# Kernel tuning notes

Hardware: AMD Instinct MI355X
Metric: run time of the kernel (lower is better)

## Reference

```python
import jax, jax.numpy as jnp
import numpy as np

B, NP, FIN = 128, 64, 2048   # graphs, nodes per graph, input feat
H, D = 8, 64                 # GAT heads, per-head dim
HD = H * D                   # 512
HID = 1024                   # Set2Set channels (concat of two 512 convs)
R2 = 16.0                    # radius^2 (r=4)
SLOPE = 0.2                  # GATConv leaky_relu slope
EPS = 0.1                    # BatchNorm eps


def setup_inputs() -> dict:
    key = jax.random.key(0)
    ks = jax.random.split(key, 20)
    s = 0.02
    inp = {}
    inp['x'] = jax.random.normal(ks[0], (B * NP, FIN), jnp.float32)
    inp['pos'] = jax.random.uniform(ks[1], (B * NP, 2), jnp.float32) * 20.0
    inp['batch'] = jnp.repeat(jnp.arange(B, dtype=jnp.int32), NP)
    # lin01: Linear(2048,2048,bias=False) + BN(2048, eps=0.1) (eval mode)
    inp['W0'] = jax.random.normal(ks[2], (FIN, 2048), jnp.float32) * s
    inp['bn0_g'] = jnp.ones((2048,), jnp.float32)
    inp['bn0_b'] = jnp.zeros((2048,), jnp.float32)
    inp['bn0_m'] = jnp.zeros((2048,), jnp.float32)
    inp['bn0_v'] = jnp.ones((2048,), jnp.float32)
    # two GATConv(2048, 64, heads=8)
    inp['Wg1'] = jax.random.normal(ks[3], (2048, HD), jnp.float32) * s
    inp['as1'] = jax.random.normal(ks[4], (H, D), jnp.float32) * s
    inp['ad1'] = jax.random.normal(ks[5], (H, D), jnp.float32) * s
    inp['b1'] = jnp.zeros((HD,), jnp.float32)
    inp['Wg2'] = jax.random.normal(ks[6], (2048, HD), jnp.float32) * s
    inp['as2'] = jax.random.normal(ks[7], (H, D), jnp.float32) * s
    inp['ad2'] = jax.random.normal(ks[8], (H, D), jnp.float32) * s
    inp['b2'] = jnp.zeros((HD,), jnp.float32)
    # Set2Set LSTM: 2 layers, input 2*HID, hidden HID
    inp['Wih0'] = jax.random.normal(ks[9], (4 * HID, 2 * HID), jnp.float32) * s
    inp['Whh0'] = jax.random.normal(ks[10], (4 * HID, HID), jnp.float32) * s
    inp['bih0'] = jnp.zeros((4 * HID,), jnp.float32)
    inp['bhh0'] = jnp.zeros((4 * HID,), jnp.float32)
    inp['Wih1'] = jax.random.normal(ks[11], (4 * HID, HID), jnp.float32) * s
    inp['Whh1'] = jax.random.normal(ks[12], (4 * HID, HID), jnp.float32) * s
    inp['bih1'] = jnp.zeros((4 * HID,), jnp.float32)
    inp['bhh1'] = jnp.zeros((4 * HID,), jnp.float32)
    # lin2: Linear(2048,1024,bias=False) + BN(1024, eps=0.1)
    inp['W2'] = jax.random.normal(ks[13], (2 * HID, HID), jnp.float32) * s
    inp['bn2_g'] = jnp.ones((HID,), jnp.float32)
    inp['bn2_b'] = jnp.zeros((HID,), jnp.float32)
    inp['bn2_m'] = jnp.zeros((HID,), jnp.float32)
    inp['bn2_v'] = jnp.ones((HID,), jnp.float32)
    # lin3: Linear(1024, 10)
    inp['W3'] = jax.random.normal(ks[14], (HID, 10), jnp.float32) * s
    inp['b3'] = jnp.zeros((10,), jnp.float32)
    return inp


def _bn(x, g, b, m, v):
    return (x - m) * jax.lax.rsqrt(v + EPS) * g + b


def _gat(xb, adj, Wg, a_src, a_dst, bias):
    # xb: [B, NP, 2048], adj: [B, NP, NP] bool (diag True = self-loops)
    h = (xb @ Wg).reshape(B, NP, H, D)
    es = jnp.einsum('bnhd,hd->bnh', h, a_src)   # source-node score
    ed = jnp.einsum('bnhd,hd->bnh', h, a_dst)   # target-node score
    # e[b, i, j, h]: edge j -> i
    e = jax.nn.leaky_relu(ed[:, :, None, :] + es[:, None, :, :], SLOPE)
    e = jnp.where(adj[..., None], e, -jnp.inf)
    alpha = jax.nn.softmax(e, axis=2)           # softmax over neighbors j
    out = jnp.einsum('bijh,bjhd->bihd', alpha, h).reshape(B, NP, HD)
    return out + bias


def _cell(inp, h, c, Wih, Whh, bih, bhh):
    z = inp @ Wih.T + h @ Whh.T + bih + bhh
    i, f, g, o = jnp.split(z, 4, axis=-1)
    c = jax.nn.sigmoid(f) * c + jax.nn.sigmoid(i) * jnp.tanh(g)
    return jax.nn.sigmoid(o) * jnp.tanh(c), c


def _forward(x, pos, W0, bn0_g, bn0_b, bn0_m, bn0_v,
             Wg1, as1, ad1, b1, Wg2, as2, ad2, b2,
             Wih0, Whh0, bih0, bhh0, Wih1, Whh1, bih1, bhh1,
             W2, bn2_g, bn2_b, bn2_m, bn2_v, W3, b3):
    # radius_graph(r=4) per graph; GATConv re-adds self-loops -> diag True
    p = pos.reshape(B, NP, 2)
    d2 = jnp.sum((p[:, :, None, :] - p[:, None, :, :]) ** 2, axis=-1)
    adj = d2 <= R2
    x = _bn(jax.nn.relu(x @ W0), bn0_g, bn0_b, bn0_m, bn0_v)  # dropout: eval
    xb = x.reshape(B, NP, 2048)
    g1 = jax.nn.relu(_gat(xb, adj, Wg1, as1, ad1, b1))
    g2 = jax.nn.relu(_gat(xb, adj, Wg2, as2, ad2, b2))
    x2 = jnp.concatenate([g1, g2], axis=-1)                   # [B, NP, 1024]
    # Set2Set: processing_steps=2, 2-layer LSTM
    q_star = jnp.zeros((B, 2 * HID), x2.dtype)
    h0 = c0 = h1 = c1 = jnp.zeros((B, HID), x2.dtype)
    for _ in range(2):
        h0, c0 = _cell(q_star, h0, c0, Wih0, Whh0, bih0, bhh0)
        h1, c1 = _cell(h0, h1, c1, Wih1, Whh1, bih1, bhh1)
        e = jnp.einsum('bnd,bd->bn', x2, h1)
        a = jax.nn.softmax(e, axis=1)                         # per-graph softmax
        r = jnp.einsum('bn,bnd->bd', a, x2)
        q_star = jnp.concatenate([h1, r], axis=-1)            # [B, 2048]
    y = _bn(jax.nn.relu(q_star @ W2), bn2_g, bn2_b, bn2_m, bn2_v)
    return y @ W3 + b3                                        # [B, 10] ('A2')


def reference(x, pos, batch, W0, bn0_g, bn0_b, bn0_m, bn0_v,
              Wg1, as1, ad1, b1, Wg2, as2, ad2, b2,
              Wih0, Whh0, bih0, bhh0, Wih1, Whh1, bih1, bhh1,
              W2, bn2_g, bn2_b, bn2_m, bn2_v, W3, b3):
    # batch ids are implicit in the fixed [B, NP] layout
    return _forward(x, pos, W0, bn0_g, bn0_b, bn0_m, bn0_v,
                    Wg1, as1, ad1, b1, Wg2, as2, ad2, b2,
                    Wih0, Whh0, bih0, bhh0, Wih1, Whh1, bih1, bhh1,
                    W2, bn2_g, bn2_b, bn2_m, bn2_v, W3, b3)
```

## Files before the change

### kernel.cpp

```cpp
#include <hip/hip_runtime.h>
#include <hip/hip_bf16.h>

typedef unsigned short u16;
typedef __attribute__((ext_vector_type(8))) short short8;
typedef __attribute__((ext_vector_type(4))) float f32x4;
typedef unsigned long long u64;

#define DI __device__ __forceinline__

DI u16 f2b(float f){
  unsigned u = __float_as_uint(f);
  unsigned r = 0x7fffu + ((u >> 16) & 1u);
  return (u16)((u + r) >> 16);
}
DI float b2f(u16 u){ return __uint_as_float((unsigned)u << 16); }

DI void gl_lds16(const void* g, void* l){
  __builtin_amdgcn_global_load_lds((const __attribute__((address_space(1))) void*)g,
                                   (__attribute__((address_space(3))) void*)l, 16, 0, 0);
}

constexpr size_t O_XBF = 0;
constexpr size_t O_W0T = O_XBF + 33554432;
constexpr size_t O_WGT = O_W0T + 8388608;
constexpr size_t O_W2T = O_WGT + 4194304;
constexpr size_t O_XB  = O_W2T + 4194304;
constexpr size_t O_H   = O_XB  + 33554432;
constexpr size_t O_ES  = O_H   + 33554432;
constexpr size_t O_ED  = O_ES  + 524288;
constexpr size_t O_ADJ = O_ED  + 524288;
constexpr size_t O_SC0 = O_ADJ + 65536;
constexpr size_t O_SH0 = O_SC0 + 8192;
constexpr size_t O_SC2 = O_SH0 + 8192;
constexpr size_t O_SH2 = O_SC2 + 4096;
constexpr size_t O_LB0 = O_SH2 + 4096;
constexpr size_t O_LB1 = O_LB0 + 16384;
constexpr size_t S_AC0 = 0;
constexpr size_t S_AC1 = S_AC0 + 786432;
constexpr size_t S_C0  = S_AC1 + 524288;
constexpr size_t S_C1  = S_C0  + 524288;
constexpr size_t S_H1F = S_C1  + 524288;
constexpr size_t S_ZP  = S_H1F + 524288;
constexpr size_t S_E   = S_ZP  + 16777216;
constexpr size_t S_Z1U = S_E   + 32768;

__global__ __launch_bounds__(256) void cvt_x(const float* __restrict__ x, u16* __restrict__ xbf){
  int idx = blockIdx.x * 256 + threadIdx.x;
  int r = idx >> 9, c4 = (idx & 511) << 2;
  float4 v = *(const float4*)(x + (size_t)r * 2048 + c4);
  u16 o[4] = { f2b(v.x), f2b(v.y), f2b(v.z), f2b(v.w) };
  *(ushort4*)(xbf + (size_t)r * 2048 + c4) = *(ushort4*)o;
}

__global__ void cvt_tr(const float* __restrict__ W0, const float* __restrict__ Wg1,
                       const float* __restrict__ Wg2, const float* __restrict__ W2,
                       u16* __restrict__ w0t, u16* __restrict__ wgt, u16* __restrict__ w2t){
  __shared__ float tile[32][33];
  int bx = blockIdx.x;
  const float* src; u16* dst; int C, droff;
  if(bx < 64){      src = W0;  dst = w0t; C = 2048; droff = 0; }
  else if(bx < 80){ src = Wg1; dst = wgt; C = 512;  droff = 0;   bx -= 64; }
  else if(bx < 96){ src = Wg2; dst = wgt; C = 512;  droff = 512; bx -= 80; }
  else {            src = W2;  dst = w2t; C = 1024; droff = 0;   bx -= 96; }
  int c0 = bx * 32, r0 = blockIdx.y * 32;
  int tx = threadIdx.x, ty = threadIdx.y;
  for(int i = 0; i < 4; i++)
    tile[ty + 8*i][tx] = src[(size_t)(r0 + ty + 8*i) * C + c0 + tx];
  __syncthreads();
  for(int i = 0; i < 4; i++)
    dst[(size_t)(droff + c0 + ty + 8*i) * 2048 + r0 + tx] = f2b(tile[tx][ty + 8*i]);
}

__global__ __launch_bounds__(256) void prep_adj(
    const float* __restrict__ g0, const float* __restrict__ b0, const float* __restrict__ m0, const float* __restrict__ v0,
    const float* __restrict__ g2, const float* __restrict__ b2, const float* __restrict__ m2, const float* __restrict__ v2,
    const float* __restrict__ bih0, const float* __restrict__ bhh0,
    const float* __restrict__ bih1, const float* __restrict__ bhh1,
    float* __restrict__ sc0, float* __restrict__ sh0, float* __restrict__ sc2, float* __restrict__ sh2,
    float* __restrict__ lb0, float* __restrict__ lb1,
    const float* __restrict__ pos, u64* __restrict__ adjm){
  int bx = blockIdx.x, tid = threadIdx.x;
  if(bx < 16){
    int t = bx * 256 + tid;
    if(t < 2048){ float s = g0[t] * rsqrtf(v0[t] + 0.1f); sc0[t] = s; sh0[t] = b0[t] - m0[t] * s; }
    if(t < 1024){ float s = g2[t] * rsqrtf(v2[t] + 0.1f); sc2[t] = s; sh2[t] = b2[t] - m2[t] * s; }
    lb0[t] = bih0[t] + bhh0[t];
    lb1[t] = bih1[t] + bhh1[t];
  } else {
    __shared__ float px[4][64], py[4][64];
    int w = tid >> 6, l = tid & 63;
    int g = (bx - 16) * 4 + w;
    float2 p = ((const float2*)pos)[g * 64 + l];
    px[w][l] = p.x; py[w][l] = p.y;
    __syncthreads();
    float xi = p.x, yi = p.y;
    u64 m = 0;
    for(int j = 0; j < 64; j++){
      float dx = xi - px[w][j], dy = yi - py[w][j];
      if(dx * dx + dy * dy <= 16.0f) m |= (1ull << j);
    }
    adjm[g * 64 + l] = m;
  }
}

template<int MODE>
__global__ __launch_bounds__(256) void gemm_bf16(
    const u16* __restrict__ A, const u16* __restrict__ Bt,
    float* __restrict__ Cf, u16* __restrict__ Cb,
    const float* __restrict__ p1, const float* __restrict__ p2,
    int M, int N, int K)
{
  constexpr int BM = 128, BN = 128, BK = 64;
  __shared__ alignas(16) u16 Al[BM * BK];
  __shared__ alignas(16) u16 Bl[BN * BK];
  int m0 = blockIdx.x * BM, n0 = blockIdx.y * BN;
  int t = threadIdx.x, w = t >> 6, l = t & 63;
  int wm = (w >> 1) * 64, wn = (w & 1) * 64;
  f32x4 acc[4][4];
  for(int a = 0; a < 4; a++) for(int b = 0; b < 4; b++) acc[a][b] = {0.f, 0.f, 0.f, 0.f};

  const short8* Ap = (const short8*)Al;
  const short8* Bp = (const short8*)Bl;

  for(int k0 = 0; k0 < K; k0 += BK){
    #pragma unroll
    for(int u = t; u < BM * 8; u += 256){
      int r = u >> 3, c = u & 7;
      gl_lds16(A + (size_t)(m0 + r) * K + k0 + ((c ^ (r & 7)) << 3), Al + u * 8);
    }
    #pragma unroll
    for(int u = t; u < BN * 8; u += 256){
      int r = u >> 3, c = u & 7;
      gl_lds16(Bt + (size_t)(n0 + r) * K + k0 + ((c ^ (r & 7)) << 3), Bl + u * 8);
    }
    __syncthreads();
    #pragma unroll
    for(int ks = 0; ks < 2; ks++){
      int kc = ks * 4 + (l >> 4);
      short8 av[4], bv[4];
      #pragma unroll
      for(int mi = 0; mi < 4; mi++){ int r = wm + mi * 16 + (l & 15); av[mi] = Ap[r * 8 + (kc ^ (r & 7))]; }
      #pragma unroll
      for(int ni = 0; ni < 4; ni++){ int r = wn + ni * 16 + (l & 15); bv[ni] = Bp[r * 8 + (kc ^ (r & 7))]; }
      #pragma unroll
      for(int mi = 0; mi < 4; mi++)
        #pragma unroll
        for(int ni = 0; ni < 4; ni++)
          acc[mi][ni] = __builtin_amdgcn_mfma_f32_16x16x32_bf16(av[mi], bv[ni], acc[mi][ni], 0, 0, 0);
    }
    __syncthreads();
  }

  int cr = m0 + wm + ((l >> 4) << 2);
  int cc = n0 + wn + (l & 15);
  for(int mi = 0; mi < 4; mi++)
    for(int ni = 0; ni < 4; ni++)
      for(int r = 0; r < 4; r++){
        int row = cr + mi * 16 + r, col = cc + ni * 16;
        float v = acc[mi][ni][r];
        if(MODE == 1){ v = fmaxf(v, 0.f) * p1[col] + p2[col]; Cb[(size_t)row * N + col] = f2b(v); }
        else if(MODE == 3){ Cb[(size_t)row * N + col] = f2b(v); }
        else { Cf[(size_t)row * N + col] = v; }
      }
}

__global__ __launch_bounds__(256) void gemm_sk(
    const u16* __restrict__ A, const u16* __restrict__ Bt, float* __restrict__ Cf,
    int N, int lda, int ldb, int kPer)
{
  constexpr int BM = 128, BN = 64, BK = 64;
  __shared__ alignas(16) u16 Al[BM * BK];
  __shared__ alignas(16) u16 Bl[BN * BK];
  int n0 = blockIdx.x * BN;
  int kb = blockIdx.y * kPer;
  float* C = Cf + (size_t)blockIdx.y * 128 * N;
  int t = threadIdx.x, w = t >> 6, l = t & 63;
  int wm = (w >> 1) * 64, wn = (w & 1) * 32;
  f32x4 acc[4][2];
  for(int a = 0; a < 4; a++) for(int b = 0; b < 2; b++) acc[a][b] = {0.f, 0.f, 0.f, 0.f};

  const short8* Ap = (const short8*)Al;
  const short8* Bp = (const short8*)Bl;

  for(int k0 = kb; k0 < kb + kPer; k0 += BK){
    #pragma unroll
    for(int u = t; u < BM * 8; u += 256){
      int r = u >> 3, c = u & 7;
      gl_lds16(A + (size_t)r * lda + k0 + ((c ^ (r & 7)) << 3), Al + u * 8);
    }
    #pragma unroll
    for(int u = t; u < BN * 8; u += 256){
      int r = u >> 3, c = u & 7;
      gl_lds16(Bt + (size_t)(n0 + r) * ldb + k0 + ((c ^ (r & 7)) << 3), Bl + u * 8);
    }
    __syncthreads();
    #pragma unroll
    for(int ks = 0; ks < 2; ks++){
      int kc = ks * 4 + (l >> 4);
      short8 av[4], bv[2];
      #pragma unroll
      for(int mi = 0; mi < 4; mi++){ int r = wm + mi * 16 + (l & 15); av[mi] = Ap[r * 8 + (kc ^ (r & 7))]; }
      #pragma unroll
      for(int ni = 0; ni < 2; ni++){ int r = wn + ni * 16 + (l & 15); bv[ni] = Bp[r * 8 + (kc ^ (r & 7))]; }
      #pragma unroll
      for(int mi = 0; mi < 4; mi++)
        #pragma unroll
        for(int ni = 0; ni < 2; ni++)
          acc[mi][ni] = __builtin_amdgcn_mfma_f32_16x16x32_bf16(av[mi], bv[ni], acc[mi][ni], 0, 0, 0);
    }
    __syncthreads();
  }

  int cr = wm + ((l >> 4) << 2);
  int cc = n0 + wn + (l & 15);
  for(int mi = 0; mi < 4; mi++)
    for(int ni = 0; ni < 2; ni++)
      for(int r = 0; r < 4; r++)
        C[(size_t)(cr + mi * 16 + r) * N + cc + ni * 16] = acc[mi][ni][r];
}

__global__ __launch_bounds__(256) void gemm_skf(
    const u16* __restrict__ A, const float* __restrict__ Wih, const float* __restrict__ Whh,
    float* __restrict__ Cf, int N, int lda, int Kih, int Khh, int kPer)
{
  constexpr int BM = 128, BN = 64, BK = 64;
  __shared__ alignas(16) u16 Al[BM * BK];
  __shared__ alignas(16) u16 Bl[BN * BK];
  int n0 = blockIdx.x * BN;
  int kb = blockIdx.y * kPer;
  float* C = Cf + (size_t)blockIdx.y * 128 * N;
  int t = threadIdx.x, w = t >> 6, l = t & 63;
  int wm = (w >> 1) * 64, wn = (w & 1) * 32;
  f32x4 acc[4][2];
  for(int a = 0; a < 4; a++) for(int b = 0; b < 2; b++) acc[a][b] = {0.f, 0.f, 0.f, 0.f};

  const short8* Ap = (const short8*)Al;
  const short8* Bp = (const short8*)Bl;

  for(int k0 = kb; k0 < kb + kPer; k0 += BK){
    #pragma unroll
    for(int u = t; u < BM * 8; u += 256){
      int r = u >> 3, c = u & 7;
      gl_lds16(A + (size_t)r * lda + k0 + ((c ^ (r & 7)) << 3), Al + u * 8);
    }
    #pragma unroll
    for(int u = t; u < BN * 8; u += 256){
      int r = u >> 3, c = u & 7;
      int gk = k0 + c * 8;
      const float* src = (gk < Kih) ? (Wih + (size_t)(n0 + r) * Kih + gk)
                                    : (Whh + (size_t)(n0 + r) * Khh + (gk - Kih));
      float4 v0 = *(const float4*)src;
      float4 v1 = *(const float4*)(src + 4);
      short8 ov;
      ov[0] = (short)f2b(v0.x); ov[1] = (short)f2b(v0.y); ov[2] = (short)f2b(v0.z); ov[3] = (short)f2b(v0.w);
      ov[4] = (short)f2b(v1.x); ov[5] = (short)f2b(v1.y); ov[6] = (short)f2b(v1.z); ov[7] = (short)f2b(v1.w);
      ((short8*)Bl)[r * 8 + (c ^ (r & 7))] = ov;
    }
    __syncthreads();
    #pragma unroll
    for(int ks = 0; ks < 2; ks++){
      int kc = ks * 4 + (l >> 4);
      short8 av[4], bv[2];
      #pragma unroll
      for(int mi = 0; mi < 4; mi++){ int r = wm + mi * 16 + (l & 15); av[mi] = Ap[r * 8 + (kc ^ (r & 7))]; }
      #pragma unroll
      for(int ni = 0; ni < 2; ni++){ int r = wn + ni * 16 + (l & 15); bv[ni] = Bp[r * 8 + (kc ^ (r & 7))]; }
      #pragma unroll
      for(int mi = 0; mi < 4; mi++)
        #pragma unroll
        for(int ni = 0; ni < 2; ni++)
          acc[mi][ni] = __builtin_amdgcn_mfma_f32_16x16x32_bf16(av[mi], bv[ni], acc[mi][ni], 0, 0, 0);
    }
    __syncthreads();
  }

  int cr = wm + ((l >> 4) << 2);
  int cc = n0 + wn + (l & 15);
  for(int mi = 0; mi < 4; mi++)
    for(int ni = 0; ni < 2; ni++)
      for(int r = 0; r < 4; r++)
        C[(size_t)(cr + mi * 16 + r) * N + cc + ni * 16] = acc[mi][ni][r];
}

__global__ __launch_bounds__(256) void gat_attn2(const u64* __restrict__ adjm,
    const u16* __restrict__ h,
    const float* __restrict__ as1, const float* __restrict__ ad1,
    const float* __restrict__ as2, const float* __restrict__ ad2,
    const float* __restrict__ b1, const float* __restrict__ b2,
    u16* __restrict__ x2b){
  int b = blockIdx.x;
  int cv = blockIdx.y >> 3, hh = blockIdx.y & 7;
  __shared__ float hst[64][64];
  __shared__ float alphaL[64][65];
  __shared__ float esl[64], edl[64];
  __shared__ u64 adjs[64];
  int t = threadIdx.x, w = t >> 6, l = t & 63;
  {
    int j = t >> 2, d0 = (t & 3) * 16;
    const u16* hr = h + (size_t)(b * 64 + j) * 1024 + cv * 512 + hh * 64 + d0;
    #pragma unroll
    for(int k = 0; k < 16; k++) hst[j][d0 + k] = b2f(hr[k]);
  }
  if(t < 64) adjs[t] = adjm[b * 64 + t];
  __syncthreads();
  float aSl = ((cv ? as2 : as1) + hh * 64)[l];
  float aDl = ((cv ? ad2 : ad1) + hh * 64)[l];
  for(int it = 0; it < 16; it++){
    int j = it * 4 + w;
    float v = hst[j][l];
    float ps = v * aSl, pd = v * aDl;
    for(int o = 32; o; o >>= 1){ ps += __shfl_xor(ps, o); pd += __shfl_xor(pd, o); }
    if(l == 0){ esl[j] = ps; edl[j] = pd; }
  }
  __syncthreads();
  for(int it = 0; it < 16; it++){
    int i = it * 4 + w;
    bool on = (adjs[i] >> l) & 1;
    float e = edl[i] + esl[l];
    e = e > 0.f ? e : 0.2f * e;
    float mx = on ? e : -1e30f;
    for(int o = 32; o; o >>= 1) mx = fmaxf(mx, __shfl_xor(mx, o));
    float p = on ? __expf(e - mx) : 0.f;
    float s = p;
    for(int o = 32; o; o >>= 1) s += __shfl_xor(s, o);
    alphaL[i][l] = p / s;
  }
  __syncthreads();
  int i = t >> 2, q = t & 3;
  float acc[16];
  #pragma unroll
  for(int k = 0; k < 16; k++) acc[k] = 0.f;
  for(int j = 0; j < 64; j++){
    float al = alphaL[i][j];
    const float* hr = &hst[j][q * 16];
    #pragma unroll
    for(int k = 0; k < 16; k++) acc[k] += al * hr[k];
  }
  const float* bias = (cv ? b2 : b1) + hh * 64 + q * 16;
  u16* op = x2b + (size_t)(b * 64 + i) * 1024 + cv * 512 + hh * 64 + q * 16;
  #pragma unroll
  for(int k = 0; k < 16; k++) op[k] = f2b(fmaxf(acc[k] + bias[k], 0.f));
}

__global__ __launch_bounds__(256) void s2s0_gemv(const float* __restrict__ Wih1,
    const float* __restrict__ lb1, const float* __restrict__ lb0, float* __restrict__ z1u){
  __shared__ float hs[1024];
  int t = threadIdx.x;
  for(int i = t; i < 1024; i += 256){
    float zi = lb0[i], zg = lb0[2048 + i], zo = lb0[3072 + i];
    float cn = (1.f / (1.f + __expf(-zi))) * tanhf(zg);
    hs[i] = (1.f / (1.f + __expf(-zo))) * tanhf(cn);
  }
  __syncthreads();
  int w = t >> 6, l = t & 63;
  int r = blockIdx.x * 4 + w;
  const float* wr = Wih1 + (size_t)r * 1024;
  float s = 0.f;
  #pragma unroll
  for(int k = 0; k < 16; k++) s += wr[l + 64 * k] * hs[l + 64 * k];
  for(int o = 32; o; o >>= 1) s += __shfl_xor(s, o);
  if(l == 0) z1u[r] = s + lb1[r];
}

__global__ void s2s0_bcast(const float* __restrict__ lb0, const float* __restrict__ z1u,
    float* __restrict__ c0b, float* __restrict__ c1b, float* __restrict__ h1f,
    u16* __restrict__ ac0, u16* __restrict__ ac1){
  int t = blockIdx.x * 256 + threadIdx.x;
  int b = t >> 10, j = t & 1023;
  float zi0 = lb0[j], zg0 = lb0[2048 + j], zo0 = lb0[3072 + j];
  float c0 = (1.f / (1.f + __expf(-zi0))) * tanhf(zg0);
  float h0 = (1.f / (1.f + __expf(-zo0))) * tanhf(c0);
  float zi1 = z1u[j], zg1 = z1u[2048 + j], zo1 = z1u[3072 + j];
  float c1 = (1.f / (1.f + __expf(-zi1))) * tanhf(zg1);
  float h1 = (1.f / (1.f + __expf(-zo1))) * tanhf(c1);
  c0b[t] = c0;
  c1b[t] = c1;
  h1f[t] = h1;
  u16 h0b = f2b(h0), h1b = f2b(h1);
  ac0[(size_t)b * 3072 + j] = h1b;
  ac0[(size_t)b * 3072 + 2048 + j] = h0b;
  ac1[(size_t)b * 2048 + j] = h0b;
  ac1[(size_t)b * 2048 + 1024 + j] = h1b;
}

__global__ void lstm_gate0(const float* __restrict__ zp, const float* __restrict__ lb,
                           float* __restrict__ c, u16* __restrict__ ac0, u16* __restrict__ ac1,
                           int ns){
  int t = blockIdx.x * 256 + threadIdx.x;
  int b = t >> 10, j = t & 1023;
  size_t base = (size_t)b * 4096;
  float zi = 0, zf = 0, zg = 0, zo = 0;
  for(int s = 0; s < ns; s++){
    const float* zr = zp + (size_t)s * 524288 + base;
    zi += zr[j]; zf += zr[1024 + j]; zg += zr[2048 + j]; zo += zr[3072 + j];
  }
  zi += lb[j]; zf += lb[1024 + j]; zg += lb[2048 + j]; zo += lb[3072 + j];
  float ci = c[t];
  float si = 1.f / (1.f + __expf(-zi)), sf = 1.f / (1.f + __expf(-zf)), so = 1.f / (1.f + __expf(-zo));
  float cn = sf * ci + si * tanhf(zg);
  c[t] = cn;
  u16 hb = f2b(so * tanhf(cn));
  ac0[(size_t)b * 3072 + 2048 + j] = hb;
  ac1[(size_t)b * 2048 + j] = hb;
}

__global__ void lstm_gate1(const float* __restrict__ zp, const float* __restrict__ lb,
                           float* __restrict__ c, float* __restrict__ h1f,
                           u16* __restrict__ ac1, u16* __restrict__ ac0, int ns){
  int t = blockIdx.x * 256 + threadIdx.x;
  int b = t >> 10, j = t & 1023;
  size_t base = (size_t)b * 4096;
  float zi = 0, zf = 0, zg = 0, zo = 0;
  for(int s = 0; s < ns; s++){
    const float* zr = zp + (size_t)s * 524288 + base;
    zi += zr[j]; zf += zr[1024 + j]; zg += zr[2048 + j]; zo += zr[3072 + j];
  }
  zi += lb[j]; zf += lb[1024 + j]; zg += lb[2048 + j]; zo += lb[3072 + j];
  float ci = c[t];
  float si = 1.f / (1.f + __expf(-zi)), sf = 1.f / (1.f + __expf(-zf)), so = 1.f / (1.f + __expf(-zo));
  float cn = sf * ci + si * tanhf(zg);
  c[t] = cn;
  float hn = so * tanhf(cn);
  h1f[t] = hn;
  u16 hb = f2b(hn);
  ac1[(size_t)b * 2048 + 1024 + j] = hb;
  ac0[(size_t)b * 3072 + j] = hb;
}

__global__ __launch_bounds__(256) void s2s_e(const u16* __restrict__ x2b,
    const float* __restrict__ h1, float* __restrict__ e){
  int t = threadIdx.x, w = t >> 6, l = t & 63;
  int node = blockIdx.x * 4 + w;
  int b = node >> 6;
  const u16* xr = x2b + (size_t)node * 1024;
  const float* hr = h1 + (size_t)b * 1024;
  float s = 0.f;
  #pragma unroll
  for(int k = 0; k < 16; k++){
    int d = k * 64 + l;
    s += b2f(xr[d]) * hr[d];
  }
  for(int o = 32; o; o >>= 1) s += __shfl_xor(s, o);
  if(l == 0) e[node] = s;
}

__global__ __launch_bounds__(256) void s2s_r(const u16* __restrict__ x2b,
    const float* __restrict__ e, u16* __restrict__ ac0){
  int b = blockIdx.x, sl = blockIdx.y;
  __shared__ float al[64];
  int t = threadIdx.x;
  if(t < 64){
    float v = e[b * 64 + t];
    float mx = v;
    for(int o = 32; o; o >>= 1) mx = fmaxf(mx, __shfl_xor(mx, o));
    float p = __expf(v - mx);
    float ss = p;
    for(int o = 32; o; o >>= 1) ss += __shfl_xor(ss, o);
    al[t] = p / ss;
  }
  __syncthreads();
  int d = sl * 256 + t;
  const u16* xp = x2b + (size_t)b * 65536 + d;
  float r = 0.f;
  #pragma unroll 8
  for(int j = 0; j < 64; j++) r += al[j] * b2f(xp[j * 1024]);
  ac0[(size_t)b * 3072 + 1024 + d] = f2b(r);
}

__global__ __launch_bounds__(256) void lin3(const float* __restrict__ zp2,
    const float* __restrict__ sc2, const float* __restrict__ sh2,
    const float* __restrict__ W3, const float* __restrict__ b3, float* __restrict__ out){
  int b = blockIdx.x;
  __shared__ float yl[1024];
  int t = threadIdx.x, w = t >> 6, l = t & 63;
  for(int d = t; d < 1024; d += 256){
    float v = 0.f;
    for(int s = 0; s < 8; s++) v += zp2[(size_t)s * 131072 + b * 1024 + d];
    yl[d] = fmaxf(v, 0.f) * sc2[d] + sh2[d];
  }
  __syncthreads();
  for(int n = w; n < 10; n += 4){
    float s = 0.f;
    for(int d = l; d < 1024; d += 64) s += yl[d] * W3[d * 10 + n];
    for(int o = 32; o; o >>= 1) s += __shfl_xor(s, o);
    if(l == 0) out[b * 10 + n] = s + b3[n];
  }
}

extern "C" void kernel_launch(void* const* d_in, const int* in_sizes, int n_in,
                              void* d_out, int out_size, void* d_ws, size_t ws_size,
                              hipStream_t stream){
  const float* x    = (const float*)d_in[0];
  const float* pos  = (const float*)d_in[1];
  const float* W0   = (const float*)d_in[3];
  const float* bn0g = (const float*)d_in[4];
  const float* bn0b = (const float*)d_in[5];
  const float* bn0m = (const float*)d_in[6];
  const float* bn0v = (const float*)d_in[7];
  const float* Wg1  = (const float*)d_in[8];
  const float* as1  = (const float*)d_in[9];
  const float* ad1  = (const float*)d_in[10];
  const float* b1   = (const float*)d_in[11];
  const float* Wg2  = (const float*)d_in[12];
  const float* as2  = (const float*)d_in[13];
  const float* ad2  = (const float*)d_in[14];
  const float* b2   = (const float*)d_in[15];
  const float* Wih0 = (const float*)d_in[16];
  const float* Whh0 = (const float*)d_in[17];
  const float* bih0 = (const float*)d_in[18];
  const float* bhh0 = (const float*)d_in[19];
  const float* Wih1 = (const float*)d_in[20];
  const float* Whh1 = (const float*)d_in[21];
  const float* bih1 = (const float*)d_in[22];
  const float* bhh1 = (const float*)d_in[23];
  const float* W2   = (const float*)d_in[24];
  const float* bn2g = (const float*)d_in[25];
  const float* bn2b = (const float*)d_in[26];
  const float* bn2m = (const float*)d_in[27];
  const float* bn2v = (const float*)d_in[28];
  const float* W3   = (const float*)d_in[29];
  const float* b3   = (const float*)d_in[30];

  char* ws = (char*)d_ws;
  u16*   xbf  = (u16*)(ws + O_XBF);
  u16*   x2b  = (u16*)(ws + O_XBF);
  u16*   w0t  = (u16*)(ws + O_W0T);
  u16*   wgt  = (u16*)(ws + O_WGT);
  u16*   w2t  = (u16*)(ws + O_W2T);
  u16*   xb   = (u16*)(ws + O_XB);
  u16*   hb   = (u16*)(ws + O_H);
  u64*   adjm = (u64*)(ws + O_ADJ);
  float* sc0  = (float*)(ws + O_SC0);
  float* sh0  = (float*)(ws + O_SH0);
  float* sc2  = (float*)(ws + O_SC2);
  float* sh2  = (float*)(ws + O_SH2);
  float* lb0  = (float*)(ws + O_LB0);
  float* lb1  = (float*)(ws + O_LB1);
  char*  s2sb = ws + O_H;
  u16*   ac0  = (u16*)(s2sb + S_AC0);
  u16*   ac1  = (u16*)(s2sb + S_AC1);
  float* c0b  = (float*)(s2sb + S_C0);
  float* c1b  = (float*)(s2sb + S_C1);
  float* h1f  = (float*)(s2sb + S_H1F);
  float* zp   = (float*)(s2sb + S_ZP);
  float* ebuf = (float*)(s2sb + S_E);
  float* z1u  = (float*)(s2sb + S_Z1U);

  prep_adj<<<48, 256, 0, stream>>>(bn0g, bn0b, bn0m, bn0v, bn2g, bn2b, bn2m, bn2v,
                                   bih0, bhh0, bih1, bhh1, sc0, sh0, sc2, sh2, lb0, lb1,
                                   pos, adjm);
  cvt_x<<<16384, 256, 0, stream>>>(x, xbf);
  cvt_tr<<<dim3(128, 64), dim3(32, 8), 0, stream>>>(W0, Wg1, Wg2, W2, w0t, wgt, w2t);

  gemm_bf16<1><<<dim3(64, 16), 256, 0, stream>>>(xbf, w0t, nullptr, xb, sc0, sh0, 8192, 2048, 2048);
  gemm_bf16<3><<<dim3(64, 8), 256, 0, stream>>>(xb, wgt, nullptr, hb, nullptr, nullptr, 8192, 1024, 2048);
  gat_attn2<<<dim3(128, 16), 256, 0, stream>>>(adjm, hb, as1, ad1, as2, ad2, b1, b2, x2b);

  s2s0_gemv<<<1024, 256, 0, stream>>>(Wih1, lb1, lb0, z1u);
  s2s0_bcast<<<512, 256, 0, stream>>>(lb0, z1u, c0b, c1b, h1f, ac0, ac1);
  s2s_e<<<2048, 256, 0, stream>>>(x2b, h1f, ebuf);
  s2s_r<<<dim3(128, 4), 256, 0, stream>>>(x2b, ebuf, ac0);

  gemm_skf<<<dim3(64, 8), 256, 0, stream>>>(ac0, Wih0, Whh0, zp, 4096, 3072, 2048, 1024, 384);
  lstm_gate0<<<512, 256, 0, stream>>>(zp, lb0, c0b, ac0, ac1, 8);
  gemm_skf<<<dim3(64, 8), 256, 0, stream>>>(ac1, Wih1, Whh1, zp, 4096, 2048, 1024, 1024, 256);
  lstm_gate1<<<512, 256, 0, stream>>>(zp, lb1, c1b, h1f, ac1, ac0, 8);
  s2s_e<<<2048, 256, 0, stream>>>(x2b, h1f, ebuf);
  s2s_r<<<dim3(128, 4), 256, 0, stream>>>(x2b, ebuf, ac0);

  gemm_sk<<<dim3(16, 8), 256, 0, stream>>>(ac0, w2t, zp, 1024, 3072, 2048, 256);
  lin3<<<128, 256, 0, stream>>>(zp, sc2, sh2, W3, b3, (float*)d_out);
}
```

Measured before the change: 308.4 us.

## Merge setup kernels into one launch and fold s2s broadcast into e/r kernels

Merges cvt_x, cvt_tr and prep_adj into a single setup_all kernel that dispatches on block index, and widens x conversion to 8 elements per thread. Removes the s2s0_bcast kernel: step-0 h1 is recomputed from z1u inside s2s_e into shared memory, and the c/h broadcast writes move into s2s_r. This cuts several kernel launches and a global round trip for h1f, at the cost of redundant gate math in every s2s_e block and a larger combined grid.

```diff
diff --git a/kernel.cpp b/kernel.cpp
--- a/kernel.cpp
+++ b/kernel.cpp
@@ -44,52 +44,56 @@
 constexpr size_t S_E   = S_ZP  + 16777216;
 constexpr size_t S_Z1U = S_E   + 32768;
 
-__global__ __launch_bounds__(256) void cvt_x(const float* __restrict__ x, u16* __restrict__ xbf){
-  int idx = blockIdx.x * 256 + threadIdx.x;
-  int r = idx >> 9, c4 = (idx & 511) << 2;
-  float4 v = *(const float4*)(x + (size_t)r * 2048 + c4);
-  u16 o[4] = { f2b(v.x), f2b(v.y), f2b(v.z), f2b(v.w) };
-  *(ushort4*)(xbf + (size_t)r * 2048 + c4) = *(ushort4*)o;
-}
-
-__global__ void cvt_tr(const float* __restrict__ W0, const float* __restrict__ Wg1,
-                       const float* __restrict__ Wg2, const float* __restrict__ W2,
-                       u16* __restrict__ w0t, u16* __restrict__ wgt, u16* __restrict__ w2t){
-  __shared__ float tile[32][33];
-  int bx = blockIdx.x;
-  const float* src; u16* dst; int C, droff;
-  if(bx < 64){      src = W0;  dst = w0t; C = 2048; droff = 0; }
-  else if(bx < 80){ src = Wg1; dst = wgt; C = 512;  droff = 0;   bx -= 64; }
-  else if(bx < 96){ src = Wg2; dst = wgt; C = 512;  droff = 512; bx -= 80; }
-  else {            src = W2;  dst = w2t; C = 1024; droff = 0;   bx -= 96; }
-  int c0 = bx * 32, r0 = blockIdx.y * 32;
-  int tx = threadIdx.x, ty = threadIdx.y;
-  for(int i = 0; i < 4; i++)
-    tile[ty + 8*i][tx] = src[(size_t)(r0 + ty + 8*i) * C + c0 + tx];
-  __syncthreads();
-  for(int i = 0; i < 4; i++)
-    dst[(size_t)(droff + c0 + ty + 8*i) * 2048 + r0 + tx] = f2b(tile[tx][ty + 8*i]);
-}
-
-__global__ __launch_bounds__(256) void prep_adj(
+__global__ __launch_bounds__(256) void setup_all(
+    const float* __restrict__ x,
+    const float* __restrict__ W0, const float* __restrict__ Wg1,
+    const float* __restrict__ Wg2, const float* __restrict__ W2,
     const float* __restrict__ g0, const float* __restrict__ b0, const float* __restrict__ m0, const float* __restrict__ v0,
     const float* __restrict__ g2, const float* __restrict__ b2, const float* __restrict__ m2, const float* __restrict__ v2,
     const float* __restrict__ bih0, const float* __restrict__ bhh0,
     const float* __restrict__ bih1, const float* __restrict__ bhh1,
+    const float* __restrict__ pos,
+    u16* __restrict__ xbf, u16* __restrict__ w0t, u16* __restrict__ wgt, u16* __restrict__ w2t,
     float* __restrict__ sc0, float* __restrict__ sh0, float* __restrict__ sc2, float* __restrict__ sh2,
-    float* __restrict__ lb0, float* __restrict__ lb1,
-    const float* __restrict__ pos, u64* __restrict__ adjm){
-  int bx = blockIdx.x, tid = threadIdx.x;
-  if(bx < 16){
-    int t = bx * 256 + tid;
-    if(t < 2048){ float s = g0[t] * rsqrtf(v0[t] + 0.1f); sc0[t] = s; sh0[t] = b0[t] - m0[t] * s; }
-    if(t < 1024){ float s = g2[t] * rsqrtf(v2[t] + 0.1f); sc2[t] = s; sh2[t] = b2[t] - m2[t] * s; }
-    lb0[t] = bih0[t] + bhh0[t];
-    lb1[t] = bih1[t] + bhh1[t];
+    float* __restrict__ lb0, float* __restrict__ lb1, u64* __restrict__ adjm)
+{
+  __shared__ float tile[32][33];
+  __shared__ float px[4][64], py[4][64];
+  int bx = blockIdx.x, t = threadIdx.x;
+  if(bx < 8192){
+    int idx = bx * 256 + t;
+    int r = idx >> 8, c8 = (idx & 255) << 3;
+    const float* src = x + (size_t)r * 2048 + c8;
+    float4 v0 = *(const float4*)src;
+    float4 v1 = *(const float4*)(src + 4);
+    short8 ov;
+    ov[0] = (short)f2b(v0.x); ov[1] = (short)f2b(v0.y); ov[2] = (short)f2b(v0.z); ov[3] = (short)f2b(v0.w);
+    ov[4] = (short)f2b(v1.x); ov[5] = (short)f2b(v1.y); ov[6] = (short)f2b(v1.z); ov[7] = (short)f2b(v1.w);
+    *(short8*)(xbf + (size_t)r * 2048 + c8) = ov;
+  } else if(bx < 16384){
+    int bx2 = bx - 8192;
+    int cx = bx2 & 127, by = bx2 >> 7;
+    const float* src; u16* dst; int C, droff;
+    if(cx < 64){      src = W0;  dst = w0t; C = 2048; droff = 0; }
+    else if(cx < 80){ src = Wg1; dst = wgt; C = 512;  droff = 0;   cx -= 64; }
+    else if(cx < 96){ src = Wg2; dst = wgt; C = 512;  droff = 512; cx -= 80; }
+    else {            src = W2;  dst = w2t; C = 1024; droff = 0;   cx -= 96; }
+    int c0 = cx * 32, r0 = by * 32;
+    int tx = t & 31, ty = t >> 5;
+    for(int i = 0; i < 4; i++)
+      tile[ty + 8*i][tx] = src[(size_t)(r0 + ty + 8*i) * C + c0 + tx];
+    __syncthreads();
+    for(int i = 0; i < 4; i++)
+      dst[(size_t)(droff + c0 + ty + 8*i) * 2048 + r0 + tx] = f2b(tile[tx][ty + 8*i]);
+  } else if(bx < 16400){
+    int tt = (bx - 16384) * 256 + t;
+    if(tt < 2048){ float s = g0[tt] * rsqrtf(v0[tt] + 0.1f); sc0[tt] = s; sh0[tt] = b0[tt] - m0[tt] * s; }
+    if(tt < 1024){ float s = g2[tt] * rsqrtf(v2[tt] + 0.1f); sc2[tt] = s; sh2[tt] = b2[tt] - m2[tt] * s; }
+    lb0[tt] = bih0[tt] + bhh0[tt];
+    lb1[tt] = bih1[tt] + bhh1[tt];
   } else {
-    __shared__ float px[4][64], py[4][64];
-    int w = tid >> 6, l = tid & 63;
-    int g = (bx - 16) * 4 + w;
+    int w = t >> 6, l = t & 63;
+    int g = (bx - 16400) * 4 + w;
     float2 p = ((const float2*)pos)[g * 64 + l];
     px[w][l] = p.x; py[w][l] = p.y;
     __syncthreads();
@@ -362,27 +366,6 @@
   if(l == 0) z1u[r] = s + lb1[r];
 }
 
-__global__ void s2s0_bcast(const float* __restrict__ lb0, const float* __restrict__ z1u,
-    float* __restrict__ c0b, float* __restrict__ c1b, float* __restrict__ h1f,
-    u16* __restrict__ ac0, u16* __restrict__ ac1){
-  int t = blockIdx.x * 256 + threadIdx.x;
-  int b = t >> 10, j = t & 1023;
-  float zi0 = lb0[j], zg0 = lb0[2048 + j], zo0 = lb0[3072 + j];
-  float c0 = (1.f / (1.f + __expf(-zi0))) * tanhf(zg0);
-  float h0 = (1.f / (1.f + __expf(-zo0))) * tanhf(c0);
-  float zi1 = z1u[j], zg1 = z1u[2048 + j], zo1 = z1u[3072 + j];
-  float c1 = (1.f / (1.f + __expf(-zi1))) * tanhf(zg1);
-  float h1 = (1.f / (1.f + __expf(-zo1))) * tanhf(c1);
-  c0b[t] = c0;
-  c1b[t] = c1;
-  h1f[t] = h1;
-  u16 h0b = f2b(h0), h1b = f2b(h1);
-  ac0[(size_t)b * 3072 + j] = h1b;
-  ac0[(size_t)b * 3072 + 2048 + j] = h0b;
-  ac1[(size_t)b * 2048 + j] = h0b;
-  ac1[(size_t)b * 2048 + 1024 + j] = h1b;
-}
-
 __global__ void lstm_gate0(const float* __restrict__ zp, const float* __restrict__ lb,
                            float* __restrict__ c, u16* __restrict__ ac0, u16* __restrict__ ac1,
                            int ns){
@@ -427,25 +410,39 @@
   ac0[(size_t)b * 3072 + j] = hb;
 }
 
+template<int STEP>
 __global__ __launch_bounds__(256) void s2s_e(const u16* __restrict__ x2b,
-    const float* __restrict__ h1, float* __restrict__ e){
+    const float* __restrict__ h1, const float* __restrict__ z1u, float* __restrict__ e){
+  __shared__ float h1s[1024];
   int t = threadIdx.x, w = t >> 6, l = t & 63;
   int node = blockIdx.x * 4 + w;
   int b = node >> 6;
+  for(int i = t; i < 1024; i += 256){
+    if(STEP == 0){
+      float zi = z1u[i], zg = z1u[2048 + i], zo = z1u[3072 + i];
+      float cn = (1.f / (1.f + __expf(-zi))) * tanhf(zg);
+      h1s[i] = (1.f / (1.f + __expf(-zo))) * tanhf(cn);
+    } else {
+      h1s[i] = h1[(size_t)b * 1024 + i];
+    }
+  }
+  __syncthreads();
   const u16* xr = x2b + (size_t)node * 1024;
-  const float* hr = h1 + (size_t)b * 1024;
   float s = 0.f;
   #pragma unroll
   for(int k = 0; k < 16; k++){
     int d = k * 64 + l;
-    s += b2f(xr[d]) * hr[d];
+    s += b2f(xr[d]) * h1s[d];
   }
   for(int o = 32; o; o >>= 1) s += __shfl_xor(s, o);
   if(l == 0) e[node] = s;
 }
 
+template<int STEP>
 __global__ __launch_bounds__(256) void s2s_r(const u16* __restrict__ x2b,
-    const float* __restrict__ e, u16* __restrict__ ac0){
+    const float* __restrict__ e, u16* __restrict__ ac0,
+    const float* __restrict__ lb0, const float* __restrict__ z1u,
+    u16* __restrict__ ac1, float* __restrict__ c0b, float* __restrict__ c1b){
   int b = blockIdx.x, sl = blockIdx.y;
   __shared__ float al[64];
   int t = threadIdx.x;
@@ -465,6 +462,21 @@
   #pragma unroll 8
   for(int j = 0; j < 64; j++) r += al[j] * b2f(xp[j * 1024]);
   ac0[(size_t)b * 3072 + 1024 + d] = f2b(r);
+  if(STEP == 0){
+    float zi0 = lb0[d], zg0 = lb0[2048 + d], zo0 = lb0[3072 + d];
+    float c0 = (1.f / (1.f + __expf(-zi0))) * tanhf(zg0);
+    float h0 = (1.f / (1.f + __expf(-zo0))) * tanhf(c0);
+    float zi1 = z1u[d], zg1 = z1u[2048 + d], zo1 = z1u[3072 + d];
+    float c1 = (1.f / (1.f + __expf(-zi1))) * tanhf(zg1);
+    float h1 = (1.f / (1.f + __expf(-zo1))) * tanhf(c1);
+    c0b[(size_t)b * 1024 + d] = c0;
+    c1b[(size_t)b * 1024 + d] = c1;
+    u16 h0b = f2b(h0), h1b = f2b(h1);
+    ac0[(size_t)b * 3072 + d] = h1b;
+    ac0[(size_t)b * 3072 + 2048 + d] = h0b;
+    ac1[(size_t)b * 2048 + d] = h0b;
+    ac1[(size_t)b * 2048 + 1024 + d] = h1b;
+  }
 }
 
 __global__ __launch_bounds__(256) void lin3(const float* __restrict__ zp2,
@@ -546,27 +558,25 @@
   float* ebuf = (float*)(s2sb + S_E);
   float* z1u  = (float*)(s2sb + S_Z1U);
 
-  prep_adj<<<48, 256, 0, stream>>>(bn0g, bn0b, bn0m, bn0v, bn2g, bn2b, bn2m, bn2v,
-                                   bih0, bhh0, bih1, bhh1, sc0, sh0, sc2, sh2, lb0, lb1,
-                                   pos, adjm);
-  cvt_x<<<16384, 256, 0, stream>>>(x, xbf);
-  cvt_tr<<<dim3(128, 64), dim3(32, 8), 0, stream>>>(W0, Wg1, Wg2, W2, w0t, wgt, w2t);
+  setup_all<<<16432, 256, 0, stream>>>(x, W0, Wg1, Wg2, W2,
+                                       bn0g, bn0b, bn0m, bn0v, bn2g, bn2b, bn2m, bn2v,
+                                       bih0, bhh0, bih1, bhh1, pos,
+                                       xbf, w0t, wgt, w2t, sc0, sh0, sc2, sh2, lb0, lb1, adjm);
 
   gemm_bf16<1><<<dim3(64, 16), 256, 0, stream>>>(xbf, w0t, nullptr, xb, sc0, sh0, 8192, 2048, 2048);
   gemm_bf16<3><<<dim3(64, 8), 256, 0, stream>>>(xb, wgt, nullptr, hb, nullptr, nullptr, 8192, 1024, 2048);
   gat_attn2<<<dim3(128, 16), 256, 0, stream>>>(adjm, hb, as1, ad1, as2, ad2, b1, b2, x2b);
 
   s2s0_gemv<<<1024, 256, 0, stream>>>(Wih1, lb1, lb0, z1u);
-  s2s0_bcast<<<512, 256, 0, stream>>>(lb0, z1u, c0b, c1b, h1f, ac0, ac1);
-  s2s_e<<<2048, 256, 0, stream>>>(x2b, h1f, ebuf);
-  s2s_r<<<dim3(128, 4), 256, 0, stream>>>(x2b, ebuf, ac0);
+  s2s_e<0><<<2048, 256, 0, stream>>>(x2b, nullptr, z1u, ebuf);
+  s2s_r<0><<<dim3(128, 4), 256, 0, stream>>>(x2b, ebuf, ac0, lb0, z1u, ac1, c0b, c1b);
 
   gemm_skf<<<dim3(64, 8), 256, 0, stream>>>(ac0, Wih0, Whh0, zp, 4096, 3072, 2048, 1024, 384);
   lstm_gate0<<<512, 256, 0, stream>>>(zp, lb0, c0b, ac0, ac1, 8);
   gemm_skf<<<dim3(64, 8), 256, 0, stream>>>(ac1, Wih1, Whh1, zp, 4096, 2048, 1024, 1024, 256);
   lstm_gate1<<<512, 256, 0, stream>>>(zp, lb1, c1b, h1f, ac1, ac0, 8);
-  s2s_e<<<2048, 256, 0, stream>>>(x2b, h1f, ebuf);
-  s2s_r<<<dim3(128, 4), 256, 0, stream>>>(x2b, ebuf, ac0);
+  s2s_e<1><<<2048, 256, 0, stream>>>(x2b, h1f, nullptr, ebuf);
+  s2s_r<1><<<dim3(128, 4), 256, 0, stream>>>(x2b, ebuf, ac0, nullptr, nullptr, nullptr, nullptr, nullptr);
 
   gemm_sk<<<dim3(16, 8), 256, 0, stream>>>(ac0, w2t, zp, 1024, 3072, 2048, 256);
   lin3<<<128, 256, 0, stream>>>(zp, sc2, sh2, W3, b3, (float*)d_out);
```

Result: no change. 303.2 us (-1.7%).
